# Kernel optimization log

Hardware: AMD Instinct MI355X
Metric: run time of the kernel (lower is better)

## Reference

```python
import jax, jax.numpy as jnp
import numpy as np

N_NODES = 100000
N_EDGES = 600000
D = 128
H = 256


def setup_inputs() -> dict:
    key = jax.random.key(0)
    ks = jax.random.split(key, 8)
    nodes = jax.random.normal(ks[0], (N_NODES, D), dtype=jnp.float32)
    senders = jax.random.randint(ks[1], (N_EDGES,), 0, N_NODES)
    receivers = jax.random.randint(ks[2], (N_EDGES,), 0, N_NODES)
    s = 0.05
    return {
        "nodes": nodes,
        "senders": senders,
        "receivers": receivers,
        "Wm1": jax.random.normal(ks[3], (D, H), dtype=jnp.float32) * s,
        "bm1": jnp.zeros((H,), dtype=jnp.float32),
        "Wm2": jax.random.normal(ks[4], (H, D), dtype=jnp.float32) * s,
        "bm2": jnp.zeros((D,), dtype=jnp.float32),
        "Wn1": jax.random.normal(ks[5], (2 * D, H), dtype=jnp.float32) * s,
        "bn1": jnp.zeros((H,), dtype=jnp.float32),
        "Wn2": jax.random.normal(ks[6], (H, D), dtype=jnp.float32) * s,
        "bn2": jnp.zeros((D,), dtype=jnp.float32),
    }


def reference(nodes, senders, receivers, Wm1, bm1, Wm2, bm2, Wn1, bn1, Wn2, bn2):
    # message MLP applied per node (vmap(message_fn) over nodes)
    m = jax.nn.relu(nodes @ Wm1 + bm1) @ Wm2 + bm2            # [N, D]
    # gather messages along edges by sender, segment_sum to receivers
    agg = jax.ops.segment_sum(m[senders], receivers, num_segments=nodes.shape[0])  # [N, D]
    # node update MLP on [nodes || aggregated messages]
    h = jnp.concatenate([nodes, agg], axis=-1)                # [N, 2D]
    upd = jax.nn.relu(h @ Wn1 + bn1) @ Wn2 + bn2              # [N, D]
    # residual add
    return nodes + upd
```

## Files before the change

kernel.cpp:

```cpp
#include <hip/hip_runtime.h>

#define NN 100000
#define DD 128
#define HH 256
#define NE 600000
#define CAP 32

typedef short bf8 __attribute__((ext_vector_type(8)));
typedef float f32x4 __attribute__((ext_vector_type(4)));
typedef unsigned short u16x8 __attribute__((ext_vector_type(8)));

__device__ __forceinline__ unsigned short f2bf(float f) {
  unsigned int u = __builtin_bit_cast(unsigned int, f);
  u += 0x7fffu + ((u >> 16) & 1u);
  return (unsigned short)(u >> 16);
}
__device__ __forceinline__ float bf2f(unsigned short h) {
  unsigned int u = ((unsigned int)h) << 16;
  return __builtin_bit_cast(float, u);
}

__global__ __launch_bounds__(256) void pack(
    const float* __restrict__ Wm1, const float* __restrict__ Wm2,
    const float* __restrict__ Wn1, const float* __restrict__ Wn2,
    unsigned short* __restrict__ Pm1, unsigned short* __restrict__ Pm2,
    unsigned short* __restrict__ Pn1, unsigned short* __restrict__ Pn2,
    int* __restrict__ cnt) {
  int b = blockIdx.x;
  int gid = b * 256 + threadIdx.x;
  for (int i = gid; i < NN; i += 80 * 256) cnt[i] = 0;

  const float* W; unsigned short* P; int K, N, base;
  if (b < 16)      { W = Wm1; P = Pm1; K = 128; N = 256; base = 0;  }
  else if (b < 32) { W = Wm2; P = Pm2; K = 256; N = 128; base = 16; }
  else if (b < 64) { W = Wn1; P = Pn1; K = 256; N = 256; base = 32; }
  else             { W = Wn2; P = Pn2; K = 256; N = 128; base = 64; }
  int idx = (b - base) * 256 + threadIdx.x;
  int KT = K >> 5;
  int lane = idx & 63;
  int t = idx >> 6;
  int kt = t % KT, nt = t / KT;
  int n = nt * 16 + (lane & 15);
  int k0 = kt * 32 + (lane >> 4) * 8;
  unsigned short* dst = P + (size_t)idx * 8;
#pragma unroll
  for (int j = 0; j < 8; ++j) dst[j] = f2bf(W[(size_t)(k0 + j) * N + n]);
}

__global__ __launch_bounds__(512) void msg_mlp(
    const float* __restrict__ nodes,
    const unsigned short* __restrict__ W1p, const float* __restrict__ b1,
    const unsigned short* __restrict__ W2p, const float* __restrict__ b2,
    unsigned short* __restrict__ Mb, unsigned short* __restrict__ Xb,
    const int* __restrict__ snd, const int* __restrict__ rcv,
    int* __restrict__ cnt, int* __restrict__ ebuf) {
  __shared__ __align__(16) unsigned short h[64][264];
  const int row0 = blockIdx.x * 64;
  const int tid = threadIdx.x;
  const int lane = tid & 63, wave = tid >> 6;
  const int l15 = lane & 15, l4 = lane >> 4;

  {
    int e = blockIdx.x * 512 + tid;
    if (e < NE) {
      int r = rcv[e];
      int pos = atomicAdd(&cnt[r], 1);
      if (pos < CAP) ebuf[r * CAP + pos] = snd[e];
    }
  }

#pragma unroll
  for (int i = 0; i < 2; ++i) {
    int flat = (i * 512 + tid) * 8;
    int r = flat >> 7, c = flat & 127;
    u16x8 o = (u16x8)0;
    if (row0 + r < NN) {
      const float4 v0 = *(const float4*)(nodes + (size_t)(row0 + r) * DD + c);
      const float4 v1 = *(const float4*)(nodes + (size_t)(row0 + r) * DD + c + 4);
      o[0] = f2bf(v0.x); o[1] = f2bf(v0.y); o[2] = f2bf(v0.z); o[3] = f2bf(v0.w);
      o[4] = f2bf(v1.x); o[5] = f2bf(v1.y); o[6] = f2bf(v1.z); o[7] = f2bf(v1.w);
      *(u16x8*)(Xb + (size_t)(row0 + r) * DD + c) = o;
    }
    *(u16x8*)&h[r][c] = o;
  }
  __syncthreads();

  f32x4 acc[2][4];
#pragma unroll
  for (int mt = 0; mt < 2; ++mt)
#pragma unroll
    for (int nt = 0; nt < 4; ++nt) acc[mt][nt] = (f32x4){0.f, 0.f, 0.f, 0.f};
#pragma unroll
  for (int kt = 0; kt < 4; ++kt) {
    bf8 wfr[2], xfr[4];
#pragma unroll
    for (int mt = 0; mt < 2; ++mt) {
      int Htile = wave * 2 + mt;
      wfr[mt] = *(const bf8*)(W1p + ((size_t)(Htile * 4 + kt) * 64 + lane) * 8);
    }
#pragma unroll
    for (int nt = 0; nt < 4; ++nt)
      xfr[nt] = *(const bf8*)&h[nt * 16 + l15][kt * 32 + l4 * 8];
#pragma unroll
    for (int mt = 0; mt < 2; ++mt)
#pragma unroll
      for (int nt = 0; nt < 4; ++nt)
        acc[mt][nt] = __builtin_amdgcn_mfma_f32_16x16x32_bf16(wfr[mt], xfr[nt], acc[mt][nt], 0, 0, 0);
  }
  __syncthreads();

#pragma unroll
  for (int mt = 0; mt < 2; ++mt) {
    int Hbase = wave * 32 + mt * 16 + l4 * 4;
    float4 bv = *(const float4*)(b1 + Hbase);
#pragma unroll
    for (int nt = 0; nt < 4; ++nt) {
      ushort4 o;
      float v0 = acc[mt][nt][0] + bv.x; o.x = f2bf(v0 > 0.f ? v0 : 0.f);
      float v1 = acc[mt][nt][1] + bv.y; o.y = f2bf(v1 > 0.f ? v1 : 0.f);
      float v2 = acc[mt][nt][2] + bv.z; o.z = f2bf(v2 > 0.f ? v2 : 0.f);
      float v3 = acc[mt][nt][3] + bv.w; o.w = f2bf(v3 > 0.f ? v3 : 0.f);
      *(ushort4*)&h[nt * 16 + l15][Hbase] = o;
    }
  }
  __syncthreads();

  f32x4 acc2[4];
#pragma unroll
  for (int nt = 0; nt < 4; ++nt) acc2[nt] = (f32x4){0.f, 0.f, 0.f, 0.f};
#pragma unroll
  for (int kt = 0; kt < 8; ++kt) {
    bf8 wfr, xfr[4];
    wfr = *(const bf8*)(W2p + ((size_t)(wave * 8 + kt) * 64 + lane) * 8);
#pragma unroll
    for (int nt = 0; nt < 4; ++nt)
      xfr[nt] = *(const bf8*)&h[nt * 16 + l15][kt * 32 + l4 * 8];
#pragma unroll
    for (int nt = 0; nt < 4; ++nt)
      acc2[nt] = __builtin_amdgcn_mfma_f32_16x16x32_bf16(wfr, xfr[nt], acc2[nt], 0, 0, 0);
  }
  {
    int Dbase = wave * 16 + l4 * 4;
    float4 bv = *(const float4*)(b2 + Dbase);
#pragma unroll
    for (int nt = 0; nt < 4; ++nt) {
      int node = row0 + nt * 16 + l15;
      if (node < NN) {
        ushort4 o;
        o.x = f2bf(acc2[nt][0] + bv.x);
        o.y = f2bf(acc2[nt][1] + bv.y);
        o.z = f2bf(acc2[nt][2] + bv.z);
        o.w = f2bf(acc2[nt][3] + bv.w);
        *(ushort4*)(Mb + (size_t)node * DD + Dbase) = o;
      }
    }
  }
}

__global__ __launch_bounds__(512) void node_fused(
    const unsigned short* __restrict__ Xb, const unsigned short* __restrict__ Mb,
    const int* __restrict__ ebuf, const int* __restrict__ cnt,
    const unsigned short* __restrict__ W1p, const float* __restrict__ b1,
    const unsigned short* __restrict__ W2p, const float* __restrict__ b2,
    float* __restrict__ out) {
  __shared__ __align__(16) unsigned short h[64][264];
  const int row0 = blockIdx.x * 64;
  const int tid = threadIdx.x;
  const int lane = tid & 63, wave = tid >> 6;
  const int l15 = lane & 15, l4 = lane >> 4;
  const int halfid = lane >> 5, sub = lane & 31;

  int degv[4], basev[4], s1[4][8];
#pragma unroll
  for (int t = 0; t < 4; ++t) {
    int node = row0 + t * 16 + wave * 2 + halfid;
    int nodec = (node < NN) ? node : 0;
    basev[t] = nodec * CAP;
    int d = (node < NN) ? cnt[node] : 0;
    degv[t] = d < CAP ? d : CAP;
  }
#pragma unroll
  for (int t = 0; t < 4; ++t)
#pragma unroll
    for (int u = 0; u < 8; ++u) s1[t][u] = ebuf[basev[t] + u];

#pragma unroll
  for (int i = 0; i < 2; ++i) {
    int flat = (i * 512 + tid) * 8;
    int r = flat >> 7, c = flat & 127;
    u16x8 v = (u16x8)0;
    if (row0 + r < NN) v = *(const u16x8*)(Xb + (size_t)(row0 + r) * DD + c);
    *(u16x8*)&h[r][c] = v;
  }

#pragma unroll
  for (int t = 0; t < 4; ++t) {
    int ln = t * 16 + wave * 2 + halfid;
    int deg = degv[t];
    float a0 = 0.f, a1 = 0.f, a2 = 0.f, a3 = 0.f;
    {
      ushort4 mv[8];
#pragma unroll
      for (int u = 0; u < 8; ++u) {
        int sl = s1[t][u];
        sl = ((unsigned)sl >= NN) ? 0 : sl;
        mv[u] = *(const ushort4*)(Mb + (size_t)sl * DD + sub * 4);
      }
#pragma unroll
      for (int u = 0; u < 8; ++u) {
        bool act = u < deg;
        a0 += act ? bf2f(mv[u].x) : 0.f;
        a1 += act ? bf2f(mv[u].y) : 0.f;
        a2 += act ? bf2f(mv[u].z) : 0.f;
        a3 += act ? bf2f(mv[u].w) : 0.f;
      }
    }
    for (int bb = 8; bb < deg; bb += 8) {
      int s[8]; ushort4 mv[8];
#pragma unroll
      for (int u = 0; u < 8; ++u) s[u] = ebuf[basev[t] + bb + u];
#pragma unroll
      for (int u = 0; u < 8; ++u) {
        int sl = s[u];
        sl = ((unsigned)sl >= NN) ? 0 : sl;
        mv[u] = *(const ushort4*)(Mb + (size_t)sl * DD + sub * 4);
      }
#pragma unroll
      for (int u = 0; u < 8; ++u) {
        bool act = (bb + u) < deg;
        a0 += act ? bf2f(mv[u].x) : 0.f;
        a1 += act ? bf2f(mv[u].y) : 0.f;
        a2 += act ? bf2f(mv[u].z) : 0.f;
        a3 += act ? bf2f(mv[u].w) : 0.f;
      }
    }
    ushort4 o;
    o.x = f2bf(a0); o.y = f2bf(a1); o.z = f2bf(a2); o.w = f2bf(a3);
    *(ushort4*)&h[ln][128 + sub * 4] = o;
  }
  __syncthreads();

  const int Dbase = wave * 16 + l4 * 4;
  ushort4 resid[4];
#pragma unroll
  for (int nt = 0; nt < 4; ++nt)
    resid[nt] = *(ushort4*)&h[nt * 16 + l15][Dbase];

  f32x4 acc[2][4];
#pragma unroll
  for (int mt = 0; mt < 2; ++mt)
#pragma unroll
    for (int nt = 0; nt < 4; ++nt) acc[mt][nt] = (f32x4){0.f, 0.f, 0.f, 0.f};
#pragma unroll
  for (int kt = 0; kt < 8; ++kt) {
    bf8 wfr[2], xfr[4];
#pragma unroll
    for (int mt = 0; mt < 2; ++mt) {
      int Htile = wave * 2 + mt;
      wfr[mt] = *(const bf8*)(W1p + ((size_t)(Htile * 8 + kt) * 64 + lane) * 8);
    }
#pragma unroll
    for (int nt = 0; nt < 4; ++nt)
      xfr[nt] = *(const bf8*)&h[nt * 16 + l15][kt * 32 + l4 * 8];
#pragma unroll
    for (int mt = 0; mt < 2; ++mt)
#pragma unroll
      for (int nt = 0; nt < 4; ++nt)
        acc[mt][nt] = __builtin_amdgcn_mfma_f32_16x16x32_bf16(wfr[mt], xfr[nt], acc[mt][nt], 0, 0, 0);
  }
  __syncthreads();

#pragma unroll
  for (int mt = 0; mt < 2; ++mt) {
    int Hbase = wave * 32 + mt * 16 + l4 * 4;
    float4 bv = *(const float4*)(b1 + Hbase);
#pragma unroll
    for (int nt = 0; nt < 4; ++nt) {
      ushort4 o;
      float v0 = acc[mt][nt][0] + bv.x; o.x = f2bf(v0 > 0.f ? v0 : 0.f);
      float v1 = acc[mt][nt][1] + bv.y; o.y = f2bf(v1 > 0.f ? v1 : 0.f);
      float v2 = acc[mt][nt][2] + bv.z; o.z = f2bf(v2 > 0.f ? v2 : 0.f);
      float v3 = acc[mt][nt][3] + bv.w; o.w = f2bf(v3 > 0.f ? v3 : 0.f);
      *(ushort4*)&h[nt * 16 + l15][Hbase] = o;
    }
  }
  __syncthreads();

  f32x4 acc2[4];
#pragma unroll
  for (int nt = 0; nt < 4; ++nt) acc2[nt] = (f32x4){0.f, 0.f, 0.f, 0.f};
#pragma unroll
  for (int kt = 0; kt < 8; ++kt) {
    bf8 wfr, xfr[4];
    wfr = *(const bf8*)(W2p + ((size_t)(wave * 8 + kt) * 64 + lane) * 8);
#pragma unroll
    for (int nt = 0; nt < 4; ++nt)
      xfr[nt] = *(const bf8*)&h[nt * 16 + l15][kt * 32 + l4 * 8];
#pragma unroll
    for (int nt = 0; nt < 4; ++nt)
      acc2[nt] = __builtin_amdgcn_mfma_f32_16x16x32_bf16(wfr, xfr[nt], acc2[nt], 0, 0, 0);
  }
  {
    float4 bv = *(const float4*)(b2 + Dbase);
#pragma unroll
    for (int nt = 0; nt < 4; ++nt) {
      int node = row0 + nt * 16 + l15;
      if (node < NN) {
        float4 o;
        o.x = bf2f(resid[nt].x) + acc2[nt][0] + bv.x;
        o.y = bf2f(resid[nt].y) + acc2[nt][1] + bv.y;
        o.z = bf2f(resid[nt].z) + acc2[nt][2] + bv.z;
        o.w = bf2f(resid[nt].w) + acc2[nt][3] + bv.w;
        *(float4*)(out + (size_t)node * DD + Dbase) = o;
      }
    }
  }
}

extern "C" void kernel_launch(void* const* d_in, const int* in_sizes, int n_in,
                              void* d_out, int out_size, void* d_ws, size_t ws_size,
                              hipStream_t stream) {
  const float* nodes = (const float*)d_in[0];
  const int* senders = (const int*)d_in[1];
  const int* receivers = (const int*)d_in[2];
  const float* Wm1 = (const float*)d_in[3];
  const float* bm1 = (const float*)d_in[4];
  const float* Wm2 = (const float*)d_in[5];
  const float* bm2 = (const float*)d_in[6];
  const float* Wn1 = (const float*)d_in[7];
  const float* bn1 = (const float*)d_in[8];
  const float* Wn2 = (const float*)d_in[9];
  const float* bn2 = (const float*)d_in[10];
  float* out = (float*)d_out;

  char* ws = (char*)d_ws;
  unsigned short* Mb   = (unsigned short*)(ws);
  unsigned short* Xb   = (unsigned short*)(ws + 25600000);
  int* cnt    = (int*)(ws + 51200000);
  int* ebuf   = (int*)(ws + 51600000);
  unsigned short* Wm1p = (unsigned short*)(ws + 64400000);
  unsigned short* Wm2p = (unsigned short*)(ws + 64465536);
  unsigned short* Wn1p = (unsigned short*)(ws + 64531072);
  unsigned short* Wn2p = (unsigned short*)(ws + 64662144);

  pack<<<80, 256, 0, stream>>>(Wm1, Wm2, Wn1, Wn2, Wm1p, Wm2p, Wn1p, Wn2p, cnt);
  msg_mlp<<<1563, 512, 0, stream>>>(nodes, Wm1p, bm1, Wm2p, bm2, Mb, Xb,
                                    senders, receivers, cnt, ebuf);
  node_fused<<<1563, 512, 0, stream>>>(Xb, Mb, ebuf, cnt,
                                       Wn1p, bn1, Wn2p, bn2, out);
}
```

Before: 227.4 us.

## Move bf16 node conversion to prep kernel and stage edge lists in LDS

The fp32-to-bf16 conversion of node features moves out of msg_mlp into an enlarged 400-block prep kernel. msg_mlp now reads the bf16 copy instead, which adds one extra full pass over the node data. node_fused loads each block's edge-sender list into shared memory with one coalesced int4 load, replacing per-thread register prefetch from global memory. It also drops the per-element masking by sending inactive slots to a zeroed sentinel row appended to Mb, which required shifting the workspace offsets.

After: 228.6 us. No clear change (+0.5%).

```diff
diff --git a/kernel.cpp b/kernel.cpp
--- a/kernel.cpp
+++ b/kernel.cpp
@@ -20,38 +20,55 @@
   return __builtin_bit_cast(float, u);
 }
 
-__global__ __launch_bounds__(256) void pack(
+__global__ __launch_bounds__(256) void prep(
     const float* __restrict__ Wm1, const float* __restrict__ Wm2,
     const float* __restrict__ Wn1, const float* __restrict__ Wn2,
     unsigned short* __restrict__ Pm1, unsigned short* __restrict__ Pm2,
     unsigned short* __restrict__ Pn1, unsigned short* __restrict__ Pn2,
-    int* __restrict__ cnt) {
+    int* __restrict__ cnt,
+    const float* __restrict__ nodes, unsigned short* __restrict__ Xb,
+    unsigned short* __restrict__ Mb) {
   int b = blockIdx.x;
   int gid = b * 256 + threadIdx.x;
-  for (int i = gid; i < NN; i += 80 * 256) cnt[i] = 0;
-
-  const float* W; unsigned short* P; int K, N, base;
-  if (b < 16)      { W = Wm1; P = Pm1; K = 128; N = 256; base = 0;  }
-  else if (b < 32) { W = Wm2; P = Pm2; K = 256; N = 128; base = 16; }
-  else if (b < 64) { W = Wn1; P = Pn1; K = 256; N = 256; base = 32; }
-  else             { W = Wn2; P = Pn2; K = 256; N = 128; base = 64; }
-  int idx = (b - base) * 256 + threadIdx.x;
-  int KT = K >> 5;
-  int lane = idx & 63;
-  int t = idx >> 6;
-  int kt = t % KT, nt = t / KT;
-  int n = nt * 16 + (lane & 15);
-  int k0 = kt * 32 + (lane >> 4) * 8;
-  unsigned short* dst = P + (size_t)idx * 8;
-#pragma unroll
-  for (int j = 0; j < 8; ++j) dst[j] = f2bf(W[(size_t)(k0 + j) * N + n]);
+
+  for (int i = gid; i < NN; i += 400 * 256) cnt[i] = 0;
+
+  if (b == 399 && threadIdx.x < 16)
+    *(u16x8*)(Mb + (size_t)NN * DD + threadIdx.x * 8) = (u16x8)0;
+
+  for (int i = gid; i < NN * DD / 8; i += 400 * 256) {
+    const float4 v0 = ((const float4*)nodes)[i * 2];
+    const float4 v1 = ((const float4*)nodes)[i * 2 + 1];
+    u16x8 o;
+    o[0] = f2bf(v0.x); o[1] = f2bf(v0.y); o[2] = f2bf(v0.z); o[3] = f2bf(v0.w);
+    o[4] = f2bf(v1.x); o[5] = f2bf(v1.y); o[6] = f2bf(v1.z); o[7] = f2bf(v1.w);
+    ((u16x8*)Xb)[i] = o;
+  }
+
+  if (b < 80) {
+    const float* W; unsigned short* P; int K, N, base;
+    if (b < 16)      { W = Wm1; P = Pm1; K = 128; N = 256; base = 0;  }
+    else if (b < 32) { W = Wm2; P = Pm2; K = 256; N = 128; base = 16; }
+    else if (b < 64) { W = Wn1; P = Pn1; K = 256; N = 256; base = 32; }
+    else             { W = Wn2; P = Pn2; K = 256; N = 128; base = 64; }
+    int idx = (b - base) * 256 + threadIdx.x;
+    int KT = K >> 5;
+    int lane = idx & 63;
+    int t = idx >> 6;
+    int kt = t % KT, nt = t / KT;
+    int n = nt * 16 + (lane & 15);
+    int k0 = kt * 32 + (lane >> 4) * 8;
+    unsigned short* dst = P + (size_t)idx * 8;
+#pragma unroll
+    for (int j = 0; j < 8; ++j) dst[j] = f2bf(W[(size_t)(k0 + j) * N + n]);
+  }
 }
 
 __global__ __launch_bounds__(512) void msg_mlp(
-    const float* __restrict__ nodes,
+    const unsigned short* __restrict__ Xb,
     const unsigned short* __restrict__ W1p, const float* __restrict__ b1,
     const unsigned short* __restrict__ W2p, const float* __restrict__ b2,
-    unsigned short* __restrict__ Mb, unsigned short* __restrict__ Xb,
+    unsigned short* __restrict__ Mb,
     const int* __restrict__ snd, const int* __restrict__ rcv,
     int* __restrict__ cnt, int* __restrict__ ebuf) {
   __shared__ __align__(16) unsigned short h[64][264];
@@ -73,15 +90,9 @@
   for (int i = 0; i < 2; ++i) {
     int flat = (i * 512 + tid) * 8;
     int r = flat >> 7, c = flat & 127;
-    u16x8 o = (u16x8)0;
-    if (row0 + r < NN) {
-      const float4 v0 = *(const float4*)(nodes + (size_t)(row0 + r) * DD + c);
-      const float4 v1 = *(const float4*)(nodes + (size_t)(row0 + r) * DD + c + 4);
-      o[0] = f2bf(v0.x); o[1] = f2bf(v0.y); o[2] = f2bf(v0.z); o[3] = f2bf(v0.w);
-      o[4] = f2bf(v1.x); o[5] = f2bf(v1.y); o[6] = f2bf(v1.z); o[7] = f2bf(v1.w);
-      *(u16x8*)(Xb + (size_t)(row0 + r) * DD + c) = o;
-    }
-    *(u16x8*)&h[r][c] = o;
+    u16x8 v = (u16x8)0;
+    if (row0 + r < NN) v = *(const u16x8*)(Xb + (size_t)(row0 + r) * DD + c);
+    *(u16x8*)&h[r][c] = v;
   }
   __syncthreads();
 
@@ -170,19 +181,21 @@
   const int l15 = lane & 15, l4 = lane >> 4;
   const int halfid = lane >> 5, sub = lane & 31;
 
-  int degv[4], basev[4], s1[4][8];
+  int degv[4];
 #pragma unroll
   for (int t = 0; t < 4; ++t) {
     int node = row0 + t * 16 + wave * 2 + halfid;
-    int nodec = (node < NN) ? node : 0;
-    basev[t] = nodec * CAP;
     int d = (node < NN) ? cnt[node] : 0;
     degv[t] = d < CAP ? d : CAP;
   }
-#pragma unroll
-  for (int t = 0; t < 4; ++t)
-#pragma unroll
-    for (int u = 0; u < 8; ++u) s1[t][u] = ebuf[basev[t] + u];
+
+  {
+    int idx = tid * 4;
+    int r = idx >> 5, s = idx & 31;
+    int4 v = (int4){0, 0, 0, 0};
+    if (row0 + r < NN) v = *(const int4*)(ebuf + (size_t)row0 * CAP + idx);
+    *(int4*)(((int*)&h[r][128]) + s) = v;
+  }
 
 #pragma unroll
   for (int i = 0; i < 2; ++i) {
@@ -192,46 +205,28 @@
     if (row0 + r < NN) v = *(const u16x8*)(Xb + (size_t)(row0 + r) * DD + c);
     *(u16x8*)&h[r][c] = v;
   }
+  __syncthreads();
 
 #pragma unroll
   for (int t = 0; t < 4; ++t) {
     int ln = t * 16 + wave * 2 + halfid;
     int deg = degv[t];
+    const int* sl_p = (const int*)&h[ln][128];
     float a0 = 0.f, a1 = 0.f, a2 = 0.f, a3 = 0.f;
-    {
+    for (int bb = 0; bb < deg; bb += 8) {
       ushort4 mv[8];
 #pragma unroll
       for (int u = 0; u < 8; ++u) {
-        int sl = s1[t][u];
-        sl = ((unsigned)sl >= NN) ? 0 : sl;
-        mv[u] = *(const ushort4*)(Mb + (size_t)sl * DD + sub * 4);
+        int s = sl_p[bb + u];
+        int se = (bb + u < deg) ? s : NN;
+        mv[u] = *(const ushort4*)(Mb + (size_t)se * DD + sub * 4);
       }
 #pragma unroll
       for (int u = 0; u < 8; ++u) {
-        bool act = u < deg;
-        a0 += act ? bf2f(mv[u].x) : 0.f;
-        a1 += act ? bf2f(mv[u].y) : 0.f;
-        a2 += act ? bf2f(mv[u].z) : 0.f;
-        a3 += act ? bf2f(mv[u].w) : 0.f;
-      }
-    }
-    for (int bb = 8; bb < deg; bb += 8) {
-      int s[8]; ushort4 mv[8];
-#pragma unroll
-      for (int u = 0; u < 8; ++u) s[u] = ebuf[basev[t] + bb + u];
-#pragma unroll
-      for (int u = 0; u < 8; ++u) {
-        int sl = s[u];
-        sl = ((unsigned)sl >= NN) ? 0 : sl;
-        mv[u] = *(const ushort4*)(Mb + (size_t)sl * DD + sub * 4);
-      }
-#pragma unroll
-      for (int u = 0; u < 8; ++u) {
-        bool act = (bb + u) < deg;
-        a0 += act ? bf2f(mv[u].x) : 0.f;
-        a1 += act ? bf2f(mv[u].y) : 0.f;
-        a2 += act ? bf2f(mv[u].z) : 0.f;
-        a3 += act ? bf2f(mv[u].w) : 0.f;
+        a0 += bf2f(mv[u].x);
+        a1 += bf2f(mv[u].y);
+        a2 += bf2f(mv[u].z);
+        a3 += bf2f(mv[u].w);
       }
     }
     ushort4 o;
@@ -335,16 +330,17 @@
 
   char* ws = (char*)d_ws;
   unsigned short* Mb   = (unsigned short*)(ws);
-  unsigned short* Xb   = (unsigned short*)(ws + 25600000);
-  int* cnt    = (int*)(ws + 51200000);
-  int* ebuf   = (int*)(ws + 51600000);
-  unsigned short* Wm1p = (unsigned short*)(ws + 64400000);
-  unsigned short* Wm2p = (unsigned short*)(ws + 64465536);
-  unsigned short* Wn1p = (unsigned short*)(ws + 64531072);
-  unsigned short* Wn2p = (unsigned short*)(ws + 64662144);
-
-  pack<<<80, 256, 0, stream>>>(Wm1, Wm2, Wn1, Wn2, Wm1p, Wm2p, Wn1p, Wn2p, cnt);
-  msg_mlp<<<1563, 512, 0, stream>>>(nodes, Wm1p, bm1, Wm2p, bm2, Mb, Xb,
+  unsigned short* Xb   = (unsigned short*)(ws + 25600512);
+  int* cnt    = (int*)(ws + 51200512);
+  int* ebuf   = (int*)(ws + 51600512);
+  unsigned short* Wm1p = (unsigned short*)(ws + 64400512);
+  unsigned short* Wm2p = (unsigned short*)(ws + 64466048);
+  unsigned short* Wn1p = (unsigned short*)(ws + 64531584);
+  unsigned short* Wn2p = (unsigned short*)(ws + 64662656);
+
+  prep<<<400, 256, 0, stream>>>(Wm1, Wm2, Wn1, Wn2, Wm1p, Wm2p, Wn1p, Wn2p,
+                                cnt, nodes, Xb, Mb);
+  msg_mlp<<<1563, 512, 0, stream>>>(Xb, Wm1p, bm1, Wm2p, bm2, Mb,
                                     senders, receivers, cnt, ebuf);
   node_fused<<<1563, 512, 0, stream>>>(Xb, Mb, ebuf, cnt,
                                        Wn1p, bn1, Wn2p, bn2, out);
```
